# Performance work log

Measured on AMD Instinct MI355X. Metric: run time of the kernel, lower is better.

## Reference

```python
import jax, jax.numpy as jnp
import numpy as np

DECAY = 0.8  # voltage decay (init arg)

# ThresholdActivation: spike = (v > 0), straight-through surrogate gradient
@jax.custom_vjp
def spike(x):
    return (x > 0).astype(x.dtype)

def _spike_fwd(x):
    return (x > 0).astype(x.dtype), None

def _spike_bwd(res, g):
    return (g,)

spike.defvjp(_spike_fwd, _spike_bwd)


def setup_inputs() -> dict:
    key = jax.random.key(0)
    k1, k2, k3 = jax.random.split(key, 3)
    B, I, H, T = 128, 512, 512, 512
    x = jax.random.normal(k1, (B, I, T), dtype=jnp.float32)
    # torch: nn.init.normal_(w, 0.1, 0.1)
    W = 0.1 + 0.1 * jax.random.normal(k2, (I, H), dtype=jnp.float32)
    b = 0.1 + 0.1 * jax.random.normal(k3, (1, H), dtype=jnp.float32)
    return {"x": x, "W": W, "b": b}


def reference(x, W, b):
    # x: (B, I, T), W: (I, H), b: (1, H)
    B, I, T = x.shape
    H = W.shape[1]
    xt = jnp.transpose(x, (2, 0, 1))              # (T, B, I)
    xw = jnp.einsum('tbi,ih->tbh', xt, W)         # batch all input matmuls: (T, B, H)

    def step(carry, xw_t):
        h, y = carry
        # s_t = relu(Wx + decay * s_{t-1} * (1 - y_{t-1}))
        h = jax.nn.relu(xw_t + DECAY * h * (1.0 - y))
        # y_t = threshold(s_t + bias)
        y = spike(h + b)
        return (h, y), y

    init = (jnp.zeros((B, H), x.dtype), jnp.zeros((B, H), x.dtype))
    _, ys = jax.lax.scan(step, init, xw)          # ys: (T, B, H)
    outputs = jnp.transpose(ys, (1, 2, 0))        # (B, H, T)
    # SNU applies SpikeActivation to the concatenated outputs
    return spike(outputs)
```

## Files before the change

kernel.cpp:

```cpp
#include <hip/hip_runtime.h>


#define DECAYF 0.8f
#define PART   ((size_t)512 * 128 * 128)

__global__ __launch_bounds__(512) void compact_cols(const float* __restrict__ bias,
                                                    int* __restrict__ hdr,
                                                    int* __restrict__ idx) {
    __shared__ unsigned long long wmask[8];
    const int tid = threadIdx.x;
    const bool p = (bias[tid] <= 0.0f);
    unsigned long long m = __ballot(p);
    const int wid = tid >> 6, lane = tid & 63;
    if (lane == 0) wmask[wid] = m;
    __syncthreads();
    int before = 0, total = 0;
    #pragma unroll
    for (int w = 0; w < 8; w++) {
        int c = __popcll(wmask[w]);
        if (w < wid) before += c;
        total += c;
    }
    if (p) idx[before + __popcll(m & ((1ull << lane) - 1ull))] = tid;
    __syncthreads();
    int idx0 = (total > 0) ? idx[0] : 0;
    if (tid >= total && tid < 256) idx[tid] = idx0;
    if (tid == 0) {
        int pc = (total + 127) & ~127;
        if (pc < 128) pc = 128;
        if (pc > 256) pc = 256;
        hdr[0] = total;
        hdr[1] = pc;
    }
}

__global__ __launch_bounds__(256) void gather_W(const float* __restrict__ W,
                                                const int* __restrict__ idx,
                                                float* __restrict__ Wc) {
    const int i = blockIdx.x;
    const int j = threadIdx.x;
    Wc[i * 256 + j] = W[i * 512 + idx[j]];
}

__global__ __launch_bounds__(256) void gemm_split(const float* __restrict__ x,
                                                  const float* __restrict__ Wc,
                                                  const int* __restrict__ hdr,
                                                  float* __restrict__ xwp,
                                                  float* __restrict__ xwc1) {
    const int kc = blockIdx.x;
    int kbeg, kend, coff;
    float* op;
    if (kc < 4) { kbeg = kc * 128; kend = kbeg + 128; coff = 0;   op = xwp + (size_t)kc * PART; }
    else        { if (hdr[1] <= 128) return;
                  kbeg = 0;        kend = 512;        coff = 128; op = xwc1; }
    const int I = 512, T = 512, NC = 256;
    const int b  = blockIdx.z;
    const int t0 = blockIdx.y * 128;

    __shared__ float As[16][132];
    __shared__ float Bs[16][132];

    const int tid  = threadIdx.x;
    const int wave = tid >> 6;
    const int lane = tid & 63;
    const int lx = lane & 7;
    const int ly = lane >> 3;
    const int m_base = ((wave >> 1) << 6) + ly * 8;
    const int n_base = ((wave & 1) << 6) + lx * 8;

    float acc[8][8];
    #pragma unroll
    for (int i = 0; i < 8; i++)
        #pragma unroll
        for (int j = 0; j < 8; j++) acc[i][j] = 0.f;

    const float* xb = x + (size_t)b * I * T;

    for (int k0 = kbeg; k0 < kend; k0 += 16) {
        #pragma unroll
        for (int j = 0; j < 2; j++) {
            int id2 = tid + j * 256;
            int row = id2 >> 5;
            int c4  = (id2 & 31) << 2;
            *(float4*)&As[row][c4] = *(const float4*)(xb + (size_t)(k0 + row) * T + t0 + c4);
            *(float4*)&Bs[row][c4] = *(const float4*)(Wc + (size_t)(k0 + row) * NC + coff + c4);
        }
        __syncthreads();
        #pragma unroll
        for (int kk = 0; kk < 16; kk++) {
            float a[8], bb[8];
            *(float4*)&a[0]  = *(const float4*)&As[kk][m_base];
            *(float4*)&a[4]  = *(const float4*)&As[kk][m_base + 4];
            *(float4*)&bb[0] = *(const float4*)&Bs[kk][n_base];
            *(float4*)&bb[4] = *(const float4*)&Bs[kk][n_base + 4];
            #pragma unroll
            for (int mi = 0; mi < 8; mi++)
                #pragma unroll
                for (int ni = 0; ni < 8; ni++)
                    acc[mi][ni] = fmaf(a[mi], bb[ni], acc[mi][ni]);
        }
        __syncthreads();
    }

    #pragma unroll
    for (int mi = 0; mi < 8; mi++) {
        int t = t0 + m_base + mi;
        float* o = op + ((size_t)t * 128 + b) * 128 + n_base;
        *(float4*)o       = *(float4*)&acc[mi][0];
        *(float4*)(o + 4) = *(float4*)&acc[mi][4];
    }
}

__global__ __launch_bounds__(256) void reduce4(float4* __restrict__ xwp4) {
    const size_t P4 = PART / 4;
    const size_t base = (size_t)blockIdx.x * 1024 + threadIdx.x;
    #pragma unroll
    for (int q = 0; q < 4; q++) {
        size_t i = base + (size_t)q * 256;
        float4 a = xwp4[i], b = xwp4[i + P4], c = xwp4[i + 2 * P4], d = xwp4[i + 3 * P4];
        float4 r;
        r.x = (a.x + b.x) + (c.x + d.x);
        r.y = (a.y + b.y) + (c.y + d.y);
        r.z = (a.z + b.z) + (c.z + d.z);
        r.w = (a.w + b.w) + (c.w + d.w);
        xwp4[i] = r;
    }
}

__global__ __launch_bounds__(256) void fill_ones(const float* __restrict__ bias,
                                                 float4* __restrict__ out4) {
    const float4 ones = make_float4(1.f, 1.f, 1.f, 1.f);
    const int base = blockIdx.x * 2048;
    #pragma unroll
    for (int q = 0; q < 8; q++) {
        int f4 = base + q * 256 + threadIdx.x;
        int h = (f4 >> 7) & 511;
        if (bias[h] > 0.0f) out4[f4] = ones;
    }
}

__global__ __launch_bounds__(128) void snu_scan(const float* __restrict__ xwp,
                                                const float* __restrict__ xwc1,
                                                const float* __restrict__ bias,
                                                const int* __restrict__ hdr,
                                                const int* __restrict__ idx,
                                                float* __restrict__ out) {
    const int T = 512;
    const int b  = blockIdx.x;
    const int jt = blockIdx.y;
    const int j  = jt * 128 + threadIdx.x;
    if (j >= hdr[0]) return;
    const int h = idx[j];
    const float bv = bias[h];
    float* o = out + ((size_t)b * 512 + h) * (size_t)T;
    const size_t STR = (size_t)128 * 128;

    const float* p = (jt == 0) ? (xwp + (size_t)b * 128 + j)
                               : (xwc1 + (size_t)b * 128 + (j - 128));

    float hs = 0.f, y = 0.f;
    float nx[8];
    #pragma unroll
    for (int d = 0; d < 8; d++) nx[d] = p[(size_t)d * STR];

    for (int t0 = 0; t0 < T; t0 += 8) {
        float cur[8], yb[8];
        #pragma unroll
        for (int d = 0; d < 8; d++) cur[d] = nx[d];
        const bool more = (t0 + 8) < T;
        #pragma unroll
        for (int d = 0; d < 8; d++)
            nx[d] = more ? p[(size_t)(t0 + 8 + d) * STR] : 0.f;
        #pragma unroll
        for (int d = 0; d < 8; d++) {
            hs = fmaf(DECAYF * hs, 1.f - y, cur[d]);
            hs = fmaxf(hs, 0.f);
            y  = (hs + bv > 0.f) ? 1.f : 0.f;
            yb[d] = y;
        }
        *(float4*)(o + t0)     = *(float4*)&yb[0];
        *(float4*)(o + t0 + 4) = *(float4*)&yb[4];
    }
}

extern "C" void kernel_launch(void* const* d_in, const int* in_sizes, int n_in,
                              void* d_out, int out_size, void* d_ws, size_t ws_size,
                              hipStream_t stream) {
    const float* x    = (const float*)d_in[0];
    const float* W    = (const float*)d_in[1];
    const float* bias = (const float*)d_in[2];
    float* out = (float*)d_out;

    char* ws = (char*)d_ws;
    int*   hdr  = (int*)(ws + 0);
    int*   idx  = (int*)(ws + 64);
    float* Wc   = (float*)(ws + 4096);
    float* xwp  = (float*)(ws + ((size_t)1 << 20));
    float* xwc1 = (float*)(ws + ((size_t)129 << 20));

    compact_cols<<<1, 512, 0, stream>>>(bias, hdr, idx);
    gather_W<<<512, 256, 0, stream>>>(W, idx, Wc);
    dim3 g1(5, 4, 128);
    gemm_split<<<g1, 256, 0, stream>>>(x, Wc, hdr, xwp, xwc1);
    reduce4<<<2048, 256, 0, stream>>>((float4*)xwp);
    fill_ones<<<4096, 256, 0, stream>>>(bias, (float4*)out);
    dim3 g2(128, 2);
    snu_scan<<<g2, 128, 0, stream>>>(xwp, xwc1, bias, hdr, idx, out);
}
```

Measured before the change: 364.4 us.

## Fuse split-K reduction and ones-fill into GEMM kernel with register prefetch

```diff
diff --git a/kernel.cpp b/kernel.cpp
--- a/kernel.cpp
+++ b/kernel.cpp
@@ -3,12 +3,15 @@
 
 #define DECAYF 0.8f
 #define PART   ((size_t)512 * 128 * 128)
+#define PARTF4 (PART / 4)
 
 __global__ __launch_bounds__(512) void compact_cols(const float* __restrict__ bias,
                                                     int* __restrict__ hdr,
-                                                    int* __restrict__ idx) {
+                                                    int* __restrict__ idx,
+                                                    int* __restrict__ cnt) {
     __shared__ unsigned long long wmask[8];
     const int tid = threadIdx.x;
+    cnt[tid] = 0;
     const bool p = (bias[tid] <= 0.0f);
     unsigned long long m = __ballot(p);
     const int wid = tid >> 6, lane = tid & 63;
@@ -42,12 +45,30 @@
     Wc[i * 256 + j] = W[i * 512 + idx[j]];
 }
 
-__global__ __launch_bounds__(256) void gemm_split(const float* __restrict__ x,
-                                                  const float* __restrict__ Wc,
-                                                  const int* __restrict__ hdr,
-                                                  float* __restrict__ xwp,
-                                                  float* __restrict__ xwc1) {
+__global__ __launch_bounds__(256) void mega(const float* __restrict__ x,
+                                            const float* __restrict__ Wc,
+                                            const int* __restrict__ hdr,
+                                            float* __restrict__ xwp,
+                                            float* __restrict__ xwc1,
+                                            const float* __restrict__ bias,
+                                            float4* __restrict__ out4,
+                                            int* __restrict__ cnt) {
     const int kc = blockIdx.x;
+    const int tid = threadIdx.x;
+
+    if (kc >= 5) {
+        const float4 ones = make_float4(1.f, 1.f, 1.f, 1.f);
+        const int fid = (kc - 5) * 512 + blockIdx.y * 128 + blockIdx.z;
+        const size_t base = (size_t)fid * 8192 + tid;
+        #pragma unroll
+        for (int q = 0; q < 32; q++) {
+            size_t f4 = base + (size_t)q * 256;
+            int h = (int)((f4 >> 7) & 511);
+            if (bias[h] > 0.0f) out4[f4] = ones;
+        }
+        return;
+    }
+
     int kbeg, kend, coff;
     float* op;
     if (kc < 4) { kbeg = kc * 128; kend = kbeg + 128; coff = 0;   op = xwp + (size_t)kc * PART; }
@@ -60,7 +81,6 @@
     __shared__ float As[16][132];
     __shared__ float Bs[16][132];
 
-    const int tid  = threadIdx.x;
     const int wave = tid >> 6;
     const int lane = tid & 63;
     const int lx = lane & 7;
@@ -75,17 +95,26 @@
         for (int j = 0; j < 8; j++) acc[i][j] = 0.f;
 
     const float* xb = x + (size_t)b * I * T;
+    const int row0 = tid >> 5,        c40 = (tid & 31) << 2;
+    const int row1 = (tid + 256) >> 5, c41 = ((tid + 256) & 31) << 2;
+
+    float4 pa0 = *(const float4*)(xb + (size_t)(kbeg + row0) * T + t0 + c40);
+    float4 pb0 = *(const float4*)(Wc + (size_t)(kbeg + row0) * NC + coff + c40);
+    float4 pa1 = *(const float4*)(xb + (size_t)(kbeg + row1) * T + t0 + c41);
+    float4 pb1 = *(const float4*)(Wc + (size_t)(kbeg + row1) * NC + coff + c41);
 
     for (int k0 = kbeg; k0 < kend; k0 += 16) {
-        #pragma unroll
-        for (int j = 0; j < 2; j++) {
-            int id2 = tid + j * 256;
-            int row = id2 >> 5;
-            int c4  = (id2 & 31) << 2;
-            *(float4*)&As[row][c4] = *(const float4*)(xb + (size_t)(k0 + row) * T + t0 + c4);
-            *(float4*)&Bs[row][c4] = *(const float4*)(Wc + (size_t)(k0 + row) * NC + coff + c4);
-        }
+        *(float4*)&As[row0][c40] = pa0;
+        *(float4*)&Bs[row0][c40] = pb0;
+        *(float4*)&As[row1][c41] = pa1;
+        *(float4*)&Bs[row1][c41] = pb1;
         __syncthreads();
+        if (k0 + 16 < kend) {
+            pa0 = *(const float4*)(xb + (size_t)(k0 + 16 + row0) * T + t0 + c40);
+            pb0 = *(const float4*)(Wc + (size_t)(k0 + 16 + row0) * NC + coff + c40);
+            pa1 = *(const float4*)(xb + (size_t)(k0 + 16 + row1) * T + t0 + c41);
+            pb1 = *(const float4*)(Wc + (size_t)(k0 + 16 + row1) * NC + coff + c41);
+        }
         #pragma unroll
         for (int kk = 0; kk < 16; kk++) {
             float a[8], bb[8];
@@ -109,33 +138,34 @@
         *(float4*)o       = *(float4*)&acc[mi][0];
         *(float4*)(o + 4) = *(float4*)&acc[mi][4];
     }
-}
-
-__global__ __launch_bounds__(256) void reduce4(float4* __restrict__ xwp4) {
-    const size_t P4 = PART / 4;
-    const size_t base = (size_t)blockIdx.x * 1024 + threadIdx.x;
-    #pragma unroll
-    for (int q = 0; q < 4; q++) {
-        size_t i = base + (size_t)q * 256;
-        float4 a = xwp4[i], b = xwp4[i + P4], c = xwp4[i + 2 * P4], d = xwp4[i + 3 * P4];
+
+    if (kc == 4) return;
+
+    __threadfence();
+    __shared__ int s_old;
+    if (tid == 0)
+        s_old = __hip_atomic_fetch_add(&cnt[blockIdx.y * 128 + blockIdx.z], 1,
+                                       __ATOMIC_ACQ_REL, __HIP_MEMORY_SCOPE_AGENT);
+    __syncthreads();
+    if (s_old != 3) return;
+    __threadfence();
+
+    float4* xwp4 = (float4*)xwp;
+    #pragma unroll
+    for (int k = 0; k < 16; k++) {
+        int f = tid + k * 256;
+        int tt = f >> 5, j4 = f & 31;
+        size_t off = ((size_t)(t0 + tt) * 128 + b) * 32 + j4;
+        float4 q0 = xwp4[off];
+        float4 q1 = xwp4[off + PARTF4];
+        float4 q2 = xwp4[off + 2 * PARTF4];
+        float4 q3 = xwp4[off + 3 * PARTF4];
         float4 r;
-        r.x = (a.x + b.x) + (c.x + d.x);
-        r.y = (a.y + b.y) + (c.y + d.y);
-        r.z = (a.z + b.z) + (c.z + d.z);
-        r.w = (a.w + b.w) + (c.w + d.w);
-        xwp4[i] = r;
-    }
-}
-
-__global__ __launch_bounds__(256) void fill_ones(const float* __restrict__ bias,
-                                                 float4* __restrict__ out4) {
-    const float4 ones = make_float4(1.f, 1.f, 1.f, 1.f);
-    const int base = blockIdx.x * 2048;
-    #pragma unroll
-    for (int q = 0; q < 8; q++) {
-        int f4 = base + q * 256 + threadIdx.x;
-        int h = (f4 >> 7) & 511;
-        if (bias[h] > 0.0f) out4[f4] = ones;
+        r.x = (q0.x + q1.x) + (q2.x + q3.x);
+        r.y = (q0.y + q1.y) + (q2.y + q3.y);
+        r.z = (q0.z + q1.z) + (q2.z + q3.z);
+        r.w = (q0.w + q1.w) + (q2.w + q3.w);
+        xwp4[off] = r;
     }
 }
 
@@ -194,16 +224,15 @@
     char* ws = (char*)d_ws;
     int*   hdr  = (int*)(ws + 0);
     int*   idx  = (int*)(ws + 64);
+    int*   cnt  = (int*)(ws + 2048);
     float* Wc   = (float*)(ws + 4096);
     float* xwp  = (float*)(ws + ((size_t)1 << 20));
     float* xwc1 = (float*)(ws + ((size_t)129 << 20));
 
-    compact_cols<<<1, 512, 0, stream>>>(bias, hdr, idx);
+    compact_cols<<<1, 512, 0, stream>>>(bias, hdr, idx, cnt);
     gather_W<<<512, 256, 0, stream>>>(W, idx, Wc);
-    dim3 g1(5, 4, 128);
-    gemm_split<<<g1, 256, 0, stream>>>(x, Wc, hdr, xwp, xwc1);
-    reduce4<<<2048, 256, 0, stream>>>((float4*)xwp);
-    fill_ones<<<4096, 256, 0, stream>>>(bias, (float4*)out);
+    dim3 g1(7, 4, 128);
+    mega<<<g1, 256, 0, stream>>>(x, Wc, hdr, xwp, xwc1, bias, (float4*)out, cnt);
     dim3 g2(128, 2);
     snu_scan<<<g2, 128, 0, stream>>>(xwp, xwc1, bias, hdr, idx, out);
 }
```

After: 1.180 ms. +223.8%, slower.

## Fuse split-K reduction, ones fill and scan into one kernel; inline column compaction

Applied to the files above, without the earlier changes.

```diff
diff --git a/kernel.cpp b/kernel.cpp
--- a/kernel.cpp
+++ b/kernel.cpp
@@ -3,56 +3,64 @@
 
 #define DECAYF 0.8f
 #define PART   ((size_t)512 * 128 * 128)
-
-__global__ __launch_bounds__(512) void compact_cols(const float* __restrict__ bias,
-                                                    int* __restrict__ hdr,
-                                                    int* __restrict__ idx) {
-    __shared__ unsigned long long wmask[8];
+#define PARTF4 (PART / 4)
+
+__device__ __forceinline__ int block_compact(const float* __restrict__ bias,
+                                             int* idx_s, int* cnt_s) {
     const int tid = threadIdx.x;
-    const bool p = (bias[tid] <= 0.0f);
-    unsigned long long m = __ballot(p);
-    const int wid = tid >> 6, lane = tid & 63;
-    if (lane == 0) wmask[wid] = m;
+    if (tid < 64) {
+        int base = 0;
+        #pragma unroll
+        for (int w = 0; w < 8; w++) {
+            bool p = bias[w * 64 + tid] <= 0.0f;
+            unsigned long long m = __ballot(p);
+            if (p) idx_s[base + __popcll(m & ((1ull << tid) - 1ull))] = w * 64 + tid;
+            base += __popcll(m);
+        }
+        if (tid == 0) cnt_s[0] = base;
+    }
     __syncthreads();
-    int before = 0, total = 0;
-    #pragma unroll
-    for (int w = 0; w < 8; w++) {
-        int c = __popcll(wmask[w]);
-        if (w < wid) before += c;
-        total += c;
-    }
-    if (p) idx[before + __popcll(m & ((1ull << lane) - 1ull))] = tid;
+    const int total = cnt_s[0];
+    const int i0 = (total > 0) ? idx_s[0] : 0;
+    for (int j = total + tid; j < 256; j += blockDim.x) idx_s[j] = i0;
     __syncthreads();
-    int idx0 = (total > 0) ? idx[0] : 0;
-    if (tid >= total && tid < 256) idx[tid] = idx0;
-    if (tid == 0) {
-        int pc = (total + 127) & ~127;
-        if (pc < 128) pc = 128;
-        if (pc > 256) pc = 256;
-        hdr[0] = total;
-        hdr[1] = pc;
-    }
-}
-
-__global__ __launch_bounds__(256) void gather_W(const float* __restrict__ W,
-                                                const int* __restrict__ idx,
+    return total;
+}
+
+__global__ __launch_bounds__(256) void gather_W(const float* __restrict__ bias,
+                                                const float* __restrict__ W,
                                                 float* __restrict__ Wc) {
+    __shared__ int idx_s[256];
+    __shared__ int cnt_s[1];
+    block_compact(bias, idx_s, cnt_s);
     const int i = blockIdx.x;
     const int j = threadIdx.x;
-    Wc[i * 256 + j] = W[i * 512 + idx[j]];
+    Wc[i * 256 + j] = W[i * 512 + idx_s[j]];
 }
 
 __global__ __launch_bounds__(256) void gemm_split(const float* __restrict__ x,
                                                   const float* __restrict__ Wc,
-                                                  const int* __restrict__ hdr,
+                                                  const float* __restrict__ bias,
                                                   float* __restrict__ xwp,
                                                   float* __restrict__ xwc1) {
     const int kc = blockIdx.x;
+    const int tid = threadIdx.x;
     int kbeg, kend, coff;
     float* op;
     if (kc < 4) { kbeg = kc * 128; kend = kbeg + 128; coff = 0;   op = xwp + (size_t)kc * PART; }
-    else        { if (hdr[1] <= 128) return;
-                  kbeg = 0;        kend = 512;        coff = 128; op = xwc1; }
+    else {
+        __shared__ int cnt_s;
+        if (tid < 64) {
+            int tot = 0;
+            #pragma unroll
+            for (int w = 0; w < 8; w++)
+                tot += __popcll(__ballot(bias[w * 64 + tid] <= 0.0f));
+            if (tid == 0) cnt_s = tot;
+        }
+        __syncthreads();
+        if (cnt_s <= 128) return;
+        kbeg = 0; kend = 512; coff = 128; op = xwc1;
+    }
     const int I = 512, T = 512, NC = 256;
     const int b  = blockIdx.z;
     const int t0 = blockIdx.y * 128;
@@ -60,7 +68,6 @@
     __shared__ float As[16][132];
     __shared__ float Bs[16][132];
 
-    const int tid  = threadIdx.x;
     const int wave = tid >> 6;
     const int lane = tid & 63;
     const int lx = lane & 7;
@@ -111,75 +118,120 @@
     }
 }
 
-__global__ __launch_bounds__(256) void reduce4(float4* __restrict__ xwp4) {
-    const size_t P4 = PART / 4;
-    const size_t base = (size_t)blockIdx.x * 1024 + threadIdx.x;
-    #pragma unroll
-    for (int q = 0; q < 4; q++) {
-        size_t i = base + (size_t)q * 256;
-        float4 a = xwp4[i], b = xwp4[i + P4], c = xwp4[i + 2 * P4], d = xwp4[i + 3 * P4];
-        float4 r;
-        r.x = (a.x + b.x) + (c.x + d.x);
-        r.y = (a.y + b.y) + (c.y + d.y);
-        r.z = (a.z + b.z) + (c.z + d.z);
-        r.w = (a.w + b.w) + (c.w + d.w);
-        xwp4[i] = r;
-    }
-}
-
-__global__ __launch_bounds__(256) void fill_ones(const float* __restrict__ bias,
-                                                 float4* __restrict__ out4) {
-    const float4 ones = make_float4(1.f, 1.f, 1.f, 1.f);
-    const int base = blockIdx.x * 2048;
-    #pragma unroll
-    for (int q = 0; q < 8; q++) {
-        int f4 = base + q * 256 + threadIdx.x;
-        int h = (f4 >> 7) & 511;
-        if (bias[h] > 0.0f) out4[f4] = ones;
-    }
-}
-
-__global__ __launch_bounds__(128) void snu_scan(const float* __restrict__ xwp,
-                                                const float* __restrict__ xwc1,
-                                                const float* __restrict__ bias,
-                                                const int* __restrict__ hdr,
-                                                const int* __restrict__ idx,
-                                                float* __restrict__ out) {
+__global__ __launch_bounds__(512) void scan_fill(const float* __restrict__ xwp,
+                                                 const float* __restrict__ xwc1,
+                                                 const float* __restrict__ bias,
+                                                 float* __restrict__ out) {
     const int T = 512;
-    const int b  = blockIdx.x;
-    const int jt = blockIdx.y;
-    const int j  = jt * 128 + threadIdx.x;
-    if (j >= hdr[0]) return;
-    const int h = idx[j];
-    const float bv = bias[h];
+    const int id  = blockIdx.x;
+    const int tid = threadIdx.x;
+
+    if (id >= 512 && id < 1536) {
+        const float4 ones = make_float4(1.f, 1.f, 1.f, 1.f);
+        float4* out4 = (float4*)out;
+        const size_t base = (size_t)(id - 512) * 8192 + tid;
+        #pragma unroll
+        for (int q = 0; q < 16; q++) {
+            size_t f4 = base + (size_t)q * 512;
+            int h = (int)((f4 >> 7) & 511);
+            if (bias[h] > 0.0f) out4[f4] = ones;
+        }
+        return;
+    }
+
+    __shared__ int idx_s[256];
+    __shared__ int cnt_s[1];
+    __shared__ float4 win[2][16][4][8];
+    const int count = block_compact(bias, idx_s, cnt_s);
+
+    if (id >= 1536) {
+        if (count <= 128) return;
+        if (tid >= count - 128) return;
+        const int b = id - 1536;
+        const int j = 128 + tid;
+        const int h = idx_s[j];
+        const float bv = bias[h];
+        const float* p = xwc1 + (size_t)b * 128 + tid;
+        float* o = out + ((size_t)b * 512 + h) * (size_t)T;
+        const size_t STR = (size_t)128 * 128;
+        float hs = 0.f, y = 0.f;
+        float nx[8];
+        #pragma unroll
+        for (int d = 0; d < 8; d++) nx[d] = p[(size_t)d * STR];
+        for (int t0 = 0; t0 < T; t0 += 8) {
+            float cur[8], yb[8];
+            #pragma unroll
+            for (int d = 0; d < 8; d++) cur[d] = nx[d];
+            const bool more = (t0 + 8) < T;
+            #pragma unroll
+            for (int d = 0; d < 8; d++)
+                nx[d] = more ? p[(size_t)(t0 + 8 + d) * STR] : 0.f;
+            #pragma unroll
+            for (int d = 0; d < 8; d++) {
+                hs = fmaf(DECAYF * hs, 1.f - y, cur[d]);
+                hs = fmaxf(hs, 0.f);
+                y  = (hs + bv > 0.f) ? 1.f : 0.f;
+                yb[d] = y;
+            }
+            *(float4*)(o + t0)     = *(float4*)&yb[0];
+            *(float4*)(o + t0 + 4) = *(float4*)&yb[4];
+        }
+        return;
+    }
+
+    const int b  = id >> 2;
+    const int jq = id & 3;
+    if (jq * 32 >= count) return;
+
+    const float4* xwp4 = (const float4*)xwp;
+    const int j4l  = tid & 7;
+    const int pp   = (tid >> 3) & 3;
+    const int toff = tid >> 5;
+    const size_t src_base = (size_t)pp * PARTF4 + (size_t)b * 32 + jq * 8 + j4l;
+
+    const int jl = tid;
+    const int j  = jq * 32 + jl;
+    const bool active = (tid < 32) && (j < count);
+    const int h = active ? idx_s[j] : 0;
+    const float bv = active ? bias[h] : 0.f;
     float* o = out + ((size_t)b * 512 + h) * (size_t)T;
-    const size_t STR = (size_t)128 * 128;
-
-    const float* p = (jt == 0) ? (xwp + (size_t)b * 128 + j)
-                               : (xwc1 + (size_t)b * 128 + (j - 128));
-
     float hs = 0.f, y = 0.f;
-    float nx[8];
-    #pragma unroll
-    for (int d = 0; d < 8; d++) nx[d] = p[(size_t)d * STR];
-
-    for (int t0 = 0; t0 < T; t0 += 8) {
-        float cur[8], yb[8];
-        #pragma unroll
-        for (int d = 0; d < 8; d++) cur[d] = nx[d];
-        const bool more = (t0 + 8) < T;
-        #pragma unroll
-        for (int d = 0; d < 8; d++)
-            nx[d] = more ? p[(size_t)(t0 + 8 + d) * STR] : 0.f;
-        #pragma unroll
-        for (int d = 0; d < 8; d++) {
-            hs = fmaf(DECAYF * hs, 1.f - y, cur[d]);
-            hs = fmaxf(hs, 0.f);
-            y  = (hs + bv > 0.f) ? 1.f : 0.f;
-            yb[d] = y;
-        }
-        *(float4*)(o + t0)     = *(float4*)&yb[0];
-        *(float4*)(o + t0 + 4) = *(float4*)&yb[4];
+
+    const float* winf = (const float*)win;
+
+    {
+        float4 v = xwp4[src_base + (size_t)toff * 128 * 32];
+        win[0][toff][pp][j4l] = v;
+    }
+    __syncthreads();
+
+    for (int w = 0; w < 32; w++) {
+        const int buf = w & 1;
+        float4 v;
+        const bool more = (w + 1) < 32;
+        if (more)
+            v = xwp4[src_base + (size_t)((w + 1) * 16 + toff) * 128 * 32];
+
+        if (active) {
+            float yb[16];
+            #pragma unroll
+            for (int d = 0; d < 16; d++) {
+                const int rb = ((buf * 16 + d) * 4) * 32 + jl;
+                float s = (winf[rb] + winf[rb + 32]) + (winf[rb + 64] + winf[rb + 96]);
+                hs = fmaf(DECAYF * hs, 1.f - y, s);
+                hs = fmaxf(hs, 0.f);
+                y  = (hs + bv > 0.f) ? 1.f : 0.f;
+                yb[d] = y;
+            }
+            const int t0 = w * 16;
+            *(float4*)(o + t0)      = *(float4*)&yb[0];
+            *(float4*)(o + t0 + 4)  = *(float4*)&yb[4];
+            *(float4*)(o + t0 + 8)  = *(float4*)&yb[8];
+            *(float4*)(o + t0 + 12) = *(float4*)&yb[12];
+        }
+        if (more)
+            win[buf ^ 1][toff][pp][j4l] = v;
+        __syncthreads();
     }
 }
 
@@ -192,18 +244,12 @@
     float* out = (float*)d_out;
 
     char* ws = (char*)d_ws;
-    int*   hdr  = (int*)(ws + 0);
-    int*   idx  = (int*)(ws + 64);
     float* Wc   = (float*)(ws + 4096);
     float* xwp  = (float*)(ws + ((size_t)1 << 20));
     float* xwc1 = (float*)(ws + ((size_t)129 << 20));
 
-    compact_cols<<<1, 512, 0, stream>>>(bias, hdr, idx);
-    gather_W<<<512, 256, 0, stream>>>(W, idx, Wc);
+    gather_W<<<512, 256, 0, stream>>>(bias, W, Wc);
     dim3 g1(5, 4, 128);
-    gemm_split<<<g1, 256, 0, stream>>>(x, Wc, hdr, xwp, xwc1);
-    reduce4<<<2048, 256, 0, stream>>>((float4*)xwp);
-    fill_ones<<<4096, 256, 0, stream>>>(bias, (float4*)out);
-    dim3 g2(128, 2);
-    snu_scan<<<g2, 128, 0, stream>>>(xwp, xwc1, bias, hdr, idx, out);
-}
+    gemm_split<<<g1, 256, 0, stream>>>(x, Wc, bias, xwp, xwc1);
+    scan_fill<<<1664, 512, 0, stream>>>(xwp, xwc1, bias, out);
+}
```

New measurement: 348.3 us. 4.4% less time.
